# Optimization experiments

Measured on AMD Instinct MI355X. Metric: run time of the kernel, lower is better.

## Reference

```python
import jax, jax.numpy as jnp
import numpy as np

# Emformer hyper-parameters (init_kwargs)
SEG = 128   # segment_length
RC = 32     # right_context_length
LC = 64     # left_context_length
MEM = 4     # max_memory_length (>0 -> 9 column groups)
N = 64      # num_segments
U = N * SEG # utterance_length (divisible by SEG => static row counts)
NUM_COLS = 9


def setup_inputs() -> dict:
    # Standard Emformer column masks: attend to own memory slot, own right-context
    # block and own (left-context-extended) segment.
    rc_q = np.array([0, 1, 0, 0, 1, 0, 0, 1, 0], dtype=bool)
    s = np.array([0, 1, 0, 0, 0, 0, 0, 1, 0], dtype=bool)
    return {
        "indices": jnp.arange(N - 1, dtype=jnp.int32)[:, None],                # (N-1, 1)
        "utt_lengths": jnp.full((N, 1), U, dtype=jnp.int32),                   # (N, 1)
        "rc_q_cols_mask_tile": jnp.asarray(np.tile(rc_q, (N - 1, 1))),         # (N-1, 9) bool
        "last_idx": jnp.full((1, 1), N - 1, dtype=jnp.int32),                  # (1, 1)
        "last_utt_lengths": jnp.full((1,), U, dtype=jnp.int32),                # (1,)
        "last_rc_q_cols_mask": jnp.asarray(rc_q[:, None]),                     # (9, 1) bool
        "s_cols_mask_tile": jnp.asarray(np.tile(s, (N - 1, 1))),               # (N-1, 9) bool
        "last_s_cols_mask": jnp.asarray(s[:, None]),                           # (9, 1) bool
    }


def _col_widths(seg_idx, num_segments, utt_len):
    """Per-segment widths of the 9 column groups. seg_idx: (N,) int32 -> (N, 9)."""
    mem_start = jnp.maximum(0, seg_idx - MEM)
    rc_start = seg_idx * RC
    seg_start = jnp.maximum(0, seg_idx * SEG - LC)
    seg_end = jnp.minimum(utt_len, (seg_idx + 1) * SEG)
    rcv = jnp.full_like(seg_idx, RC)
    return jnp.stack([
        mem_start, seg_idx - mem_start, (num_segments - 1) - seg_idx,   # memory blocks
        rc_start, rcv, RC * num_segments - (rc_start + RC),             # right-context blocks
        seg_start, seg_end - seg_start, utt_len - seg_end,              # utterance blocks
    ], axis=1)


def reference(indices, utt_lengths, rc_q_cols_mask_tile, last_idx,
              last_utt_lengths, last_rc_q_cols_mask,
              s_cols_mask_tile, last_s_cols_mask):
    # Stack all N segments (map_fn segments + the explicit last segment).
    seg_idx = jnp.concatenate([indices[:, 0], last_idx[0]]).astype(jnp.int32)          # (N,)
    rc_masks = jnp.concatenate([rc_q_cols_mask_tile,
                                jnp.transpose(last_rc_q_cols_mask)], axis=0)          # (N, 9) bool
    s_masks = jnp.concatenate([s_cols_mask_tile,
                               jnp.transpose(last_s_cols_mask)], axis=0)              # (N, 9) bool

    W = (N - 1) + RC * N + U                         # total mask width (constant per row)
    widths = _col_widths(seg_idx, N, U)              # (N, 9)
    cum_end = jnp.cumsum(widths, axis=1)             # (N, 9), last column == W

    # For each segment row, map each column j to its column-group index:
    # grp[i, j] = #{k : cum_end[i, k] <= j}  (zero-width groups are skipped correctly).
    j = jnp.arange(W, dtype=jnp.int32)
    grp = jnp.sum(j[None, :, None] >= cum_end[:, None, :], axis=-1)  # (N, W) in [0, 8]

    rc_vals = jnp.take_along_axis(rc_masks, grp, axis=1)  # (N, W) bool: 1-blocks vs 0-blocks
    s_vals = jnp.take_along_axis(s_masks, grp, axis=1)    # (N, W) bool

    # rc block: RC identical rows per segment; query block: SEG rows per segment
    # (U == N * SEG, so min(SEG, U - i*SEG) == SEG for every segment);
    # summary block: 1 row per segment.
    rc_block = jnp.repeat(rc_vals, RC, axis=0)   # (RC*N, W)
    q_block = jnp.repeat(rc_vals, SEG, axis=0)   # (U, W)
    full = jnp.concatenate([rc_block, q_block, s_vals], axis=0)  # (RC*N + U + N, W) bool

    # Original: attention_mask = (1 - mask) > 0, i.e. True where attention is disallowed.
    return jnp.logical_not(full)
```

## Files before the change

### kernel.cpp

```cpp
#include <hip/hip_runtime.h>

namespace {
constexpr int SEG  = 128;
constexpr int RCL  = 32;
constexpr int LC   = 64;
constexpr int MEM  = 4;
constexpr int NSEG = 64;
constexpr int U    = NSEG * SEG;
constexpr int W    = (NSEG - 1) + RCL * NSEG + U;
constexpr int RC_ROWS = RCL * NSEG;
constexpr int Q_ROWS  = U;
constexpr int ROWS    = RC_ROWS + Q_ROWS + NSEG;
constexpr unsigned TOTAL  = (unsigned)ROWS * (unsigned)W;
constexpr unsigned TOTAL4 = TOTAL / 4u;
constexpr int UTT_BASE = (NSEG - 1) + RCL * NSEG;
}

typedef int i32x4 __attribute__((ext_vector_type(4)));

__device__ __forceinline__ void row_params(int r, int& a0, int& a1, int& b0,
                                           int& b1, int& d0, int& d1) {
    int i;
    bool is_s;
    if (r < RC_ROWS) {
        i = r >> 5;
        is_s = false;
    } else if (r < RC_ROWS + Q_ROWS) {
        i = (r - RC_ROWS) >> 7;
        is_s = false;
    } else {
        i = r - (RC_ROWS + Q_ROWS);
        is_s = true;
    }
    a0 = max(i - MEM, 0);
    a1 = i;
    if (is_s) { b0 = 0; b1 = 0; }
    else      { b0 = (NSEG - 1) + RCL * i; b1 = b0 + RCL; }
    d0 = UTT_BASE + max(SEG * i - LC, 0);
    d1 = UTT_BASE + SEG * (i + 1);
}

__device__ __forceinline__ int mask_at(int j, int a0, int a1, int b0, int b1,
                                       int d0, int d1) {
    bool allowed = (j >= a0 && j < a1) | (j >= b0 && j < b1) | (j >= d0 && j < d1);
    return allowed ? 0 : 1;
}

__global__ __launch_bounds__(256) void emformer_mask_kernel(i32x4* __restrict__ out) {
    unsigned t = blockIdx.x * 256u + threadIdx.x;
    if (t >= TOTAL4) return;
    unsigned f = t * 4u;
    unsigned r = f / (unsigned)W;
    int j = (int)(f - r * (unsigned)W);

    i32x4 v;
    if (j + 3 < W) {
        int a0, a1, b0, b1, d0, d1;
        row_params((int)r, a0, a1, b0, b1, d0, d1);
        v.x = mask_at(j,     a0, a1, b0, b1, d0, d1);
        v.y = mask_at(j + 1, a0, a1, b0, b1, d0, d1);
        v.z = mask_at(j + 2, a0, a1, b0, b1, d0, d1);
        v.w = mask_at(j + 3, a0, a1, b0, b1, d0, d1);
    } else {
#pragma unroll
        for (int k = 0; k < 4; ++k) {
            int jj = j + k;
            int rr = (int)r;
            if (jj >= W) { jj -= W; rr += 1; }
            int a0, a1, b0, b1, d0, d1;
            row_params(rr, a0, a1, b0, b1, d0, d1);
            v[k] = mask_at(jj, a0, a1, b0, b1, d0, d1);
        }
    }
    out[t] = v;
}

extern "C" void kernel_launch(void* const* d_in, const int* in_sizes, int n_in,
                              void* d_out, int out_size, void* d_ws, size_t ws_size,
                              hipStream_t stream) {
    (void)d_in; (void)in_sizes; (void)n_in; (void)d_ws; (void)ws_size; (void)out_size;
    i32x4* out = (i32x4*)d_out;
    const unsigned blocks = (TOTAL4 + 255u) / 256u;
    emformer_mask_kernel<<<dim3(blocks), dim3(256), 0, stream>>>(out);
}
```

Before: 413.1 us.

## Compute mask row values once per segment and replicate across rows

The kernel is restructured so that each block owns one segment, one column tile and one row group. It computes the mask values for its columns once in registers and writes them to all rc and query rows of that segment, plus the summary row. This removes the per-element division, the row-parameter recomputation and the row-wrap handling. In exchange the stores become scalar 4-byte writes instead of 16-byte vector stores, and the grid is small (2048 blocks), so write bandwidth efficiency may suffer.

Result: slower. 483.1 us (+17.0%).

```diff
diff --git a/kernel.cpp b/kernel.cpp
--- a/kernel.cpp
+++ b/kernel.cpp
@@ -8,78 +8,76 @@
 constexpr int NSEG = 64;
 constexpr int U    = NSEG * SEG;
 constexpr int W    = (NSEG - 1) + RCL * NSEG + U;
-constexpr int RC_ROWS = RCL * NSEG;
-constexpr int Q_ROWS  = U;
-constexpr int ROWS    = RC_ROWS + Q_ROWS + NSEG;
-constexpr unsigned TOTAL  = (unsigned)ROWS * (unsigned)W;
-constexpr unsigned TOTAL4 = TOTAL / 4u;
+constexpr int RC_ROWS  = RCL * NSEG;
+constexpr int SUM_BASE = RC_ROWS + U;
 constexpr int UTT_BASE = (NSEG - 1) + RCL * NSEG;
+
+constexpr int COL_TILES  = 4;
+constexpr int CPT        = 2576;
+constexpr int ROW_GROUPS = 8;
+constexpr int KMAX       = 11;
 }
 
-typedef int i32x4 __attribute__((ext_vector_type(4)));
+__global__ __launch_bounds__(256) void emformer_mask_kernel(int* __restrict__ out) {
+    const int tid = (int)threadIdx.x;
+    const int rg  = (int)blockIdx.x;
+    const int ct  = (int)blockIdx.y;
+    const int i   = (int)blockIdx.z;
 
-__device__ __forceinline__ void row_params(int r, int& a0, int& a1, int& b0,
-                                           int& b1, int& d0, int& d1) {
-    int i;
-    bool is_s;
-    if (r < RC_ROWS) {
-        i = r >> 5;
-        is_s = false;
-    } else if (r < RC_ROWS + Q_ROWS) {
-        i = (r - RC_ROWS) >> 7;
-        is_s = false;
-    } else {
-        i = r - (RC_ROWS + Q_ROWS);
-        is_s = true;
+    const int colbase = ct * CPT;
+    const int ncols   = min(CPT, W - colbase);
+
+    const int a0 = max(i - MEM, 0);
+    const int a1 = i;
+    const int b0 = (NSEG - 1) + RCL * i;
+    const int d0 = UTT_BASE + max(SEG * i - LC, 0);
+    const int d1 = UTT_BASE + SEG * (i + 1);
+
+    int vq[KMAX], vs[KMAX];
+#pragma unroll
+    for (int k = 0; k < KMAX; ++k) {
+        const int c = colbase + tid + (k << 8);
+        const bool inA = (unsigned)(c - a0) < (unsigned)(a1 - a0);
+        const bool inB = (unsigned)(c - b0) < (unsigned)RCL;
+        const bool inD = (unsigned)(c - d0) < (unsigned)(d1 - d0);
+        vq[k] = (inA | inB | inD) ? 0 : 1;
+        vs[k] = (inA | inD) ? 0 : 1;
     }
-    a0 = max(i - MEM, 0);
-    a1 = i;
-    if (is_s) { b0 = 0; b1 = 0; }
-    else      { b0 = (NSEG - 1) + RCL * i; b1 = b0 + RCL; }
-    d0 = UTT_BASE + max(SEG * i - LC, 0);
-    d1 = UTT_BASE + SEG * (i + 1);
-}
 
-__device__ __forceinline__ int mask_at(int j, int a0, int a1, int b0, int b1,
-                                       int d0, int d1) {
-    bool allowed = (j >= a0 && j < a1) | (j >= b0 && j < b1) | (j >= d0 && j < d1);
-    return allowed ? 0 : 1;
-}
+    const bool has_tail = tid < (ncols - (KMAX - 1) * 256);
 
-__global__ __launch_bounds__(256) void emformer_mask_kernel(i32x4* __restrict__ out) {
-    unsigned t = blockIdx.x * 256u + threadIdx.x;
-    if (t >= TOTAL4) return;
-    unsigned f = t * 4u;
-    unsigned r = f / (unsigned)W;
-    int j = (int)(f - r * (unsigned)W);
+    int* __restrict__ p = out + (size_t)colbase + tid;
 
-    i32x4 v;
-    if (j + 3 < W) {
-        int a0, a1, b0, b1, d0, d1;
-        row_params((int)r, a0, a1, b0, b1, d0, d1);
-        v.x = mask_at(j,     a0, a1, b0, b1, d0, d1);
-        v.y = mask_at(j + 1, a0, a1, b0, b1, d0, d1);
-        v.z = mask_at(j + 2, a0, a1, b0, b1, d0, d1);
-        v.w = mask_at(j + 3, a0, a1, b0, b1, d0, d1);
-    } else {
+    {
+        const int r0 = RCL * i + rg * 4;
+        for (int rr = 0; rr < 4; ++rr) {
+            int* __restrict__ rowp = p + (size_t)(r0 + rr) * W;
 #pragma unroll
-        for (int k = 0; k < 4; ++k) {
-            int jj = j + k;
-            int rr = (int)r;
-            if (jj >= W) { jj -= W; rr += 1; }
-            int a0, a1, b0, b1, d0, d1;
-            row_params(rr, a0, a1, b0, b1, d0, d1);
-            v[k] = mask_at(jj, a0, a1, b0, b1, d0, d1);
+            for (int k = 0; k < KMAX - 1; ++k) rowp[k << 8] = vq[k];
+            if (has_tail) rowp[(KMAX - 1) << 8] = vq[KMAX - 1];
         }
     }
-    out[t] = v;
+    {
+        const int r0 = RC_ROWS + SEG * i + rg * 16;
+        for (int rr = 0; rr < 16; ++rr) {
+            int* __restrict__ rowp = p + (size_t)(r0 + rr) * W;
+#pragma unroll
+            for (int k = 0; k < KMAX - 1; ++k) rowp[k << 8] = vq[k];
+            if (has_tail) rowp[(KMAX - 1) << 8] = vq[KMAX - 1];
+        }
+    }
+    if (rg == 0) {
+        int* __restrict__ rowp = p + (size_t)(SUM_BASE + i) * W;
+#pragma unroll
+        for (int k = 0; k < KMAX - 1; ++k) rowp[k << 8] = vs[k];
+        if (has_tail) rowp[(KMAX - 1) << 8] = vs[KMAX - 1];
+    }
 }
 
 extern "C" void kernel_launch(void* const* d_in, const int* in_sizes, int n_in,
                               void* d_out, int out_size, void* d_ws, size_t ws_size,
                               hipStream_t stream) {
     (void)d_in; (void)in_sizes; (void)n_in; (void)d_ws; (void)ws_size; (void)out_size;
-    i32x4* out = (i32x4*)d_out;
-    const unsigned blocks = (TOTAL4 + 255u) / 256u;
-    emformer_mask_kernel<<<dim3(blocks), dim3(256), 0, stream>>>(out);
+    emformer_mask_kernel<<<dim3(ROW_GROUPS, COL_TILES, NSEG), dim3(256), 0, stream>>>(
+        (int*)d_out);
 }
```

## Fill mask with memset then scatter zeros for allowed column ranges

Applied to the files above, without the earlier changes.

Instead of computing every mask element in a kernel, the launch now fills the whole output with ones using hipMemsetD32Async, then runs one block per row that writes zeros only into the three allowed column ranges (memory, right-context and utterance windows). This removes the per-element range tests and leaves the bulk fill to a bandwidth-bound memset. The cost is a second launch and a few sparse, partly unaligned stores that overwrite data the memset has just written.

After: 428.6 us. +3.8%, slower.

```diff
diff --git a/kernel.cpp b/kernel.cpp
--- a/kernel.cpp
+++ b/kernel.cpp
@@ -8,78 +8,45 @@
 constexpr int NSEG = 64;
 constexpr int U    = NSEG * SEG;
 constexpr int W    = (NSEG - 1) + RCL * NSEG + U;
-constexpr int RC_ROWS = RCL * NSEG;
-constexpr int Q_ROWS  = U;
-constexpr int ROWS    = RC_ROWS + Q_ROWS + NSEG;
-constexpr unsigned TOTAL  = (unsigned)ROWS * (unsigned)W;
-constexpr unsigned TOTAL4 = TOTAL / 4u;
+constexpr int RC_ROWS  = RCL * NSEG;
+constexpr int Q_ROWS   = U;
+constexpr int ROWS     = RC_ROWS + Q_ROWS + NSEG;
 constexpr int UTT_BASE = (NSEG - 1) + RCL * NSEG;
+constexpr size_t TOTAL = (size_t)ROWS * (size_t)W;
 }
 
-typedef int i32x4 __attribute__((ext_vector_type(4)));
+__global__ __launch_bounds__(256) void emformer_zero_kernel(int* __restrict__ out) {
+    const int r = (int)blockIdx.x;
+    const int t = (int)threadIdx.x;
 
-__device__ __forceinline__ void row_params(int r, int& a0, int& a1, int& b0,
-                                           int& b1, int& d0, int& d1) {
     int i;
-    bool is_s;
+    bool is_summary = false;
     if (r < RC_ROWS) {
         i = r >> 5;
-        is_s = false;
     } else if (r < RC_ROWS + Q_ROWS) {
         i = (r - RC_ROWS) >> 7;
-        is_s = false;
     } else {
         i = r - (RC_ROWS + Q_ROWS);
-        is_s = true;
+        is_summary = true;
     }
-    a0 = max(i - MEM, 0);
-    a1 = i;
-    if (is_s) { b0 = 0; b1 = 0; }
-    else      { b0 = (NSEG - 1) + RCL * i; b1 = b0 + RCL; }
-    d0 = UTT_BASE + max(SEG * i - LC, 0);
-    d1 = UTT_BASE + SEG * (i + 1);
-}
 
-__device__ __forceinline__ int mask_at(int j, int a0, int a1, int b0, int b1,
-                                       int d0, int d1) {
-    bool allowed = (j >= a0 && j < a1) | (j >= b0 && j < b1) | (j >= d0 && j < d1);
-    return allowed ? 0 : 1;
-}
+    const int a0  = max(i - MEM, 0);
+    const int wA  = i - a0;
+    const int b0  = (NSEG - 1) + RCL * i;
+    const int d0s = max(SEG * i - LC, 0);
+    const int d0  = UTT_BASE + d0s;
+    const int wD  = SEG * (i + 1) - d0s;
 
-__global__ __launch_bounds__(256) void emformer_mask_kernel(i32x4* __restrict__ out) {
-    unsigned t = blockIdx.x * 256u + threadIdx.x;
-    if (t >= TOTAL4) return;
-    unsigned f = t * 4u;
-    unsigned r = f / (unsigned)W;
-    int j = (int)(f - r * (unsigned)W);
-
-    i32x4 v;
-    if (j + 3 < W) {
-        int a0, a1, b0, b1, d0, d1;
-        row_params((int)r, a0, a1, b0, b1, d0, d1);
-        v.x = mask_at(j,     a0, a1, b0, b1, d0, d1);
-        v.y = mask_at(j + 1, a0, a1, b0, b1, d0, d1);
-        v.z = mask_at(j + 2, a0, a1, b0, b1, d0, d1);
-        v.w = mask_at(j + 3, a0, a1, b0, b1, d0, d1);
-    } else {
-#pragma unroll
-        for (int k = 0; k < 4; ++k) {
-            int jj = j + k;
-            int rr = (int)r;
-            if (jj >= W) { jj -= W; rr += 1; }
-            int a0, a1, b0, b1, d0, d1;
-            row_params(rr, a0, a1, b0, b1, d0, d1);
-            v[k] = mask_at(jj, a0, a1, b0, b1, d0, d1);
-        }
-    }
-    out[t] = v;
+    int* __restrict__ row = out + (size_t)r * (size_t)W;
+    if (t < wA)                row[a0 + t] = 0;
+    if (!is_summary && t < RCL) row[b0 + t] = 0;
+    if (t < wD)                row[d0 + t] = 0;
 }
 
 extern "C" void kernel_launch(void* const* d_in, const int* in_sizes, int n_in,
                               void* d_out, int out_size, void* d_ws, size_t ws_size,
                               hipStream_t stream) {
     (void)d_in; (void)in_sizes; (void)n_in; (void)d_ws; (void)ws_size; (void)out_size;
-    i32x4* out = (i32x4*)d_out;
-    const unsigned blocks = (TOTAL4 + 255u) / 256u;
-    emformer_mask_kernel<<<dim3(blocks), dim3(256), 0, stream>>>(out);
+    (void)hipMemsetD32Async((hipDeviceptr_t)d_out, 1, TOTAL, stream);
+    emformer_zero_kernel<<<dim3(ROWS), dim3(256), 0, stream>>>((int*)d_out);
 }
```
